# Performance work log

Measured on AMD Instinct MI355X. Metric: run time of the kernel, lower is better.

## Reference

```python
import jax, jax.numpy as jnp
import numpy as np

KERNEL = 7  # median blur window size (odd)


def setup_inputs() -> dict:
    key = jax.random.key(0)
    # NCHW image batch, values in [0,1) like normalized images
    img = jax.random.uniform(key, (8, 3, 512, 512), dtype=jnp.float32)
    return {"img": img}


def _median_blur(img, k):
    # Matches kornia.filters.median_blur: zero padding ('same'), then median
    # over the k*k window. k*k is odd so the exact middle of the sorted
    # window equals torch.median's lower median.
    pad = k // 2
    b, c, h, w = img.shape
    x = jnp.pad(img, ((0, 0), (0, 0), (pad, pad), (pad, pad)))  # zero pad
    # unfold: [B, C, k*k, H, W] — same materialization as kornia's conv2d
    # with binary one-hot kernels. Loop is over the fixed k*k = 49 taps.
    patches = jnp.stack(
        [x[:, :, i:i + h, j:j + w] for i in range(k) for j in range(k)],
        axis=2,
    )
    mid = (k * k) // 2
    return jnp.sort(patches, axis=2)[:, :, mid]  # [B, C, H, W]


def reference(img):
    return _median_blur(img, KERNEL)
```

## Files before the change

### kernel.cpp

```cpp
#include <hip/hip_runtime.h>
#include <utility>

#define IMG_H 512
#define IMG_W 512

typedef _Float16 h2 __attribute__((ext_vector_type(2)));

__device__ __forceinline__ h2 h2min(h2 a, h2 b) { return __builtin_elementwise_min(a, b); }
__device__ __forceinline__ h2 h2max(h2 a, h2 b) { return __builtin_elementwise_max(a, b); }

struct Op { int kind, a, b; };
constexpr int NSLOT = 352;
constexpr int MAXOPS = 4096;
constexpr int NCOLREG = 70;
struct Prog { Op ops[MAXOPS]; int n; int nphys; bool ok; bool noload; };

constexpr int pow2ceil(int x) { int p = 1; while (p < x) p += p; return p; }

struct Builder {
    Op ops[MAXOPS] = {};
    int n = 0;
    bool pad[NSLOT] = {};
    bool init[NSLOT] = {};
    bool ok = true;

    constexpr void emit(int k, int a, int b) {
        if (n < MAXOPS) ops[n++] = Op{k, a, b}; else ok = false;
    }
    constexpr void load(int s, int c) { emit(2, s, c); pad[s] = false; init[s] = true; }
    constexpr void mov(int d, int s) {
        if (!init[s] || d == s) ok = false;
        emit(1, d, s); pad[d] = pad[s]; init[d] = true;
    }
    constexpr void mkpad(int s) { pad[s] = true; init[s] = true; }
    constexpr void ce_(int a, int b) {
        if (!init[a] || !init[b]) { ok = false; return; }
        if (pad[a] && pad[b]) return;
        if (!pad[a] && pad[b]) return;
        if (pad[a] && !pad[b]) {
            emit(1, a, b); pad[a] = false; pad[b] = true; return;
        }
        emit(0, a, b);
    }
    constexpr void maxin(int a, int b) {
        if (!init[a] || !init[b] || pad[a] || pad[b]) ok = false;
        emit(5, a, b);
    }
    constexpr void minin(int a, int b) {
        if (!init[a] || !init[b] || pad[a] || pad[b]) ok = false;
        emit(4, a, b);
    }
    constexpr void sort_run(int base, int len) {
        for (int p = 1; p < len; p += p)
            for (int k = p; k > 0; k /= 2)
                for (int j = k % p; j + k < len; j += k + k)
                    for (int i = 0; i < k; ++i)
                        if (i + j + k < len)
                            if ((i + j) / (p + p) == (i + j + k) / (p + p))
                                ce_(base + i + j, base + i + j + k);
    }
    constexpr void merge_stage(int base, int P) {
        int nn = 2 * P, p = P;
        for (int k = p; k > 0; k /= 2)
            for (int j = k % p; j + k < nn; j += k + k)
                for (int i = 0; i < k; ++i) {
                    int a = i + j, b = i + j + k;
                    if (b < nn && a / (p + p) == b / (p + p)) ce_(base + a, base + b);
                }
    }
    constexpr void load_col(int base, int c) {
        for (int r = 0; r < 7; ++r) load(base + r, c * 7 + r);
        sort_run(base, 7);
    }
    constexpr void place(int dst, int src, int len, int P) {
        for (int i = 0; i < len; ++i) mov(dst + i, src + i);
        for (int i = len; i < P; ++i) mkpad(dst + i);
    }
    constexpr void merge_to(int dst, int s1, int l1, int s2, int l2) {
        int P = pow2ceil(l1 > l2 ? l1 : l2);
        place(dst, s1, l1, P);
        place(dst + P, s2, l2, P);
        merge_stage(dst, P);
    }
    constexpr void select_med49(int T, int A, int B, int o) {
        for (int t = 0; t < 7; ++t) {
            mov(T + t, A + 17 + t);
            maxin(B + 6 - t, T + t);
        }
        mov(T + 7, A + 24);
        minin(T, T + 1); minin(T + 2, T + 3);
        minin(T + 4, T + 5); minin(T + 6, T + 7);
        minin(T, T + 2); minin(T + 4, T + 6);
        minin(T, T + 4);
        if (!init[T] || pad[T]) ok = false;
        emit(3, o, T);
    }
};

constexpr Prog build() {
    Builder b{};
    constexpr int M12 = 112, M34 = 128, M56 = 144, M78 = 160;
    constexpr int C28A = 208, C42 = 272, T0 = 336, T1 = 344;

    for (int c = 1; c <= 8; ++c) b.load_col(8 * c, c);
    b.merge_to(M34, 8 * 3, 7, 8 * 4, 7);
    b.merge_to(M56, 8 * 5, 7, 8 * 6, 7);
    b.merge_to(C28A, M34, 14, M56, 14);
    b.merge_to(M12, 8 * 1, 7, 8 * 2, 7);
    b.merge_to(M78, 8 * 7, 7, 8 * 8, 7);

    b.merge_to(C42, C28A, 28, M12, 14);
    b.load_col(8 * 0, 0);
    b.select_med49(T0, C42, 8 * 0, 0);
    b.select_med49(T1, C42, 8 * 7, 1);

    b.merge_to(C42, C28A, 28, M78, 14);
    b.load_col(8 * 9, 9);
    b.select_med49(T0, C42, 8 * 2, 2);
    b.select_med49(T1, C42, 8 * 9, 3);

    Prog p{};
    bool needed[NSLOT] = {};
    int kindr[MAXOPS] = {};
    bool keep[MAXOPS] = {};
    for (int t = b.n - 1; t >= 0; --t) {
        Op o = b.ops[t];
        if (o.kind == 3) { keep[t] = true; kindr[t] = 3; needed[o.b] = true; }
        else if (o.kind == 0) {
            bool na = needed[o.a], nb = needed[o.b];
            if (na && nb)      { keep[t] = true; kindr[t] = 0; }
            else if (na)       { keep[t] = true; kindr[t] = 4; needed[o.b] = true; }
            else if (nb)       { keep[t] = true; kindr[t] = 5; needed[o.a] = true; }
        } else if (o.kind == 1) {
            if (needed[o.a]) { keep[t] = true; kindr[t] = 1; needed[o.a] = false; needed[o.b] = true; }
        } else if (o.kind == 2) {
            if (needed[o.a]) { keep[t] = true; kindr[t] = 2; needed[o.a] = false; }
        } else if (o.kind == 4) {
            if (needed[o.a]) { keep[t] = true; kindr[t] = 4; needed[o.b] = true; }
        } else if (o.kind == 5) {
            if (needed[o.b]) { keep[t] = true; kindr[t] = 5; needed[o.a] = true; }
        }
    }
    p.n = 0;
    for (int t = 0; t < b.n; ++t)
        if (keep[t]) { p.ops[p.n] = b.ops[t]; p.ops[p.n].kind = kindr[t]; ++p.n; }
    p.ok = b.ok;

    bool live[NSLOT] = {};
    bool lu_a[MAXOPS] = {};
    bool lu_b[MAXOPS] = {};
    for (int t = p.n - 1; t >= 0; --t) {
        Op o = p.ops[t];
        if (o.kind == 0 || o.kind == 4 || o.kind == 5) {
            lu_a[t] = !live[o.a]; lu_b[t] = !live[o.b];
        } else if (o.kind == 1 || o.kind == 3) {
            lu_b[t] = !live[o.b];
        }
        if (o.kind == 0) { live[o.a] = false; live[o.b] = false; }
        else if (o.kind == 1 || o.kind == 2 || o.kind == 4) live[o.a] = false;
        else if (o.kind == 5) live[o.b] = false;
        if (o.kind == 0 || o.kind == 4 || o.kind == 5) { live[o.a] = true; live[o.b] = true; }
        else if (o.kind == 1 || o.kind == 3) live[o.b] = true;
    }
    for (int t = 0; t < p.n; ++t) {
        Op o = p.ops[t];
        if (o.kind == 0 && (lu_a[t] || lu_b[t])) p.ok = false;
        if (o.kind == 4 && lu_a[t]) p.ok = false;
        if (o.kind == 5 && lu_b[t]) p.ok = false;
    }

    int phys[NSLOT] = {};
    bool bound[NSLOT] = {};
    bool claimed[NCOLREG] = {};
    int freelist[NSLOT] = {};
    bool drop[MAXOPS] = {};
    int nfree = 0, nphys = NCOLREG;
    for (int t = 0; t < p.n; ++t) {
        Op o = p.ops[t];
        if (o.kind == 0) {
            if (!bound[o.a] || !bound[o.b]) p.ok = false;
            p.ops[t].a = phys[o.a]; p.ops[t].b = phys[o.b];
        } else if (o.kind == 4) {
            if (!bound[o.a] || !bound[o.b]) p.ok = false;
            p.ops[t].a = phys[o.a]; p.ops[t].b = phys[o.b];
            if (lu_b[t]) { freelist[nfree++] = phys[o.b]; bound[o.b] = false; }
        } else if (o.kind == 5) {
            if (!bound[o.a] || !bound[o.b]) p.ok = false;
            p.ops[t].a = phys[o.a]; p.ops[t].b = phys[o.b];
            if (lu_a[t]) { freelist[nfree++] = phys[o.a]; bound[o.a] = false; }
        } else if (o.kind == 1) {
            if (!bound[o.b]) p.ok = false;
            int pb = phys[o.b];
            if (lu_b[t]) {
                if (bound[o.a]) { freelist[nfree++] = phys[o.a]; bound[o.a] = false; }
                phys[o.a] = pb; bound[o.a] = true; bound[o.b] = false;
                drop[t] = true;
            } else {
                p.ops[t].b = pb;
                if (bound[o.a]) { freelist[nfree++] = phys[o.a]; bound[o.a] = false; }
                int pa = (nfree > 0) ? freelist[--nfree] : nphys++;
                phys[o.a] = pa; bound[o.a] = true;
                p.ops[t].a = pa;
            }
        } else if (o.kind == 2) {
            if (o.b < 0 || o.b >= NCOLREG || claimed[o.b]) p.ok = false;
            else claimed[o.b] = true;
            if (bound[o.a]) { freelist[nfree++] = phys[o.a]; bound[o.a] = false; }
            phys[o.a] = o.b; bound[o.a] = true;
            drop[t] = true;
        } else {
            if (!bound[o.b]) p.ok = false;
            p.ops[t].b = phys[o.b];
            if (lu_b[t]) { freelist[nfree++] = phys[o.b]; bound[o.b] = false; }
        }
        if (nphys > NSLOT || nfree > NSLOT) p.ok = false;
    }
    p.nphys = nphys;

    int m = 0;
    p.noload = true;
    for (int t = 0; t < p.n; ++t) {
        if (drop[t]) continue;
        if (p.ops[t].kind == 2) p.noload = false;
        p.ops[m++] = p.ops[t];
    }
    p.n = m;
    return p;
}

constexpr Prog PROG = build();
static_assert(PROG.ok && PROG.n > 0 && PROG.n < 2000, "program build failed");
static_assert(PROG.noload, "a load op survived precoloring");
static_assert(PROG.nphys >= NCOLREG && PROG.nphys <= 256, "regalloc blew up");
constexpr int NPHYS = PROG.nphys;

template <int I>
__device__ __forceinline__ void step(h2* v, h2* med) {
    constexpr Op o = PROG.ops[I];
    if constexpr (o.kind == 0) {
        h2 lo = h2min(v[o.a], v[o.b]);
        h2 hi = h2max(v[o.a], v[o.b]);
        v[o.a] = lo; v[o.b] = hi;
    } else if constexpr (o.kind == 1) v[o.a] = v[o.b];
    else if constexpr (o.kind == 3) med[o.a] = v[o.b];
    else if constexpr (o.kind == 4) v[o.a] = h2min(v[o.a], v[o.b]);
    else v[o.b] = h2max(v[o.a], v[o.b]);
}

template <size_t... Is>
__device__ __forceinline__ void run_all(h2* v, h2* med, std::index_sequence<Is...>) {
    (step<(int)Is>(v, med), ...);
}

__global__ __launch_bounds__(256, 2) void median7x7_kernel(
        const float* __restrict__ img, float* __restrict__ out) {
    const int bc = blockIdx.z;
    const int tx = threadIdx.x;
    const int ty = threadIdx.y;
    const int x0 = (blockIdx.x * 64 + tx) * 4;
    const int y  = (blockIdx.y * 4 + ty) * 2;

    const float* base = img + (size_t)bc * (IMG_H * IMG_W);
    const bool okl = (x0 >= 4);
    const bool okr = (x0 <= 504);
    const int xl = okl ? (x0 - 4) : 0;
    const int xr = okr ? (x0 + 4) : 504;

    h2 v[NPHYS];
    float prv[10];
#pragma unroll
    for (int r = 0; r < 8; ++r) {
        const int yy = y - 3 + r;
        float4 Q0, Q1, Q2;
        if ((unsigned)yy < IMG_H) {
            const float* rp = base + (size_t)yy * IMG_W;
            Q0 = *(const float4*)(rp + xl);
            Q1 = *(const float4*)(rp + x0);
            Q2 = *(const float4*)(rp + xr);
        } else {
            Q0 = make_float4(0.f, 0.f, 0.f, 0.f); Q1 = Q0; Q2 = Q0;
        }
        float cur[10];
        cur[0] = okl ? Q0.y : 0.f; cur[1] = okl ? Q0.z : 0.f; cur[2] = okl ? Q0.w : 0.f;
        cur[3] = Q1.x; cur[4] = Q1.y; cur[5] = Q1.z; cur[6] = Q1.w;
        cur[7] = okr ? Q2.x : 0.f; cur[8] = okr ? Q2.y : 0.f; cur[9] = okr ? Q2.z : 0.f;
        if (r > 0) {
#pragma unroll
            for (int c = 0; c < 10; ++c)
                v[c * 7 + (r - 1)] = (h2)__builtin_amdgcn_cvt_pkrtz(prv[c], cur[c]);
        }
#pragma unroll
        for (int c = 0; c < 10; ++c) prv[c] = cur[c];
    }

    h2 med[4];
    run_all(v, med, std::make_index_sequence<(size_t)PROG.n>{});

    float* op = out + (size_t)bc * (IMG_H * IMG_W) + (size_t)y * IMG_W + x0;
    *(float4*)op = make_float4((float)med[0].x, (float)med[1].x,
                               (float)med[2].x, (float)med[3].x);
    *(float4*)(op + IMG_W) = make_float4((float)med[0].y, (float)med[1].y,
                                         (float)med[2].y, (float)med[3].y);
}

extern "C" void kernel_launch(void* const* d_in, const int* in_sizes, int n_in,
                              void* d_out, int out_size, void* d_ws, size_t ws_size,
                              hipStream_t stream) {
    const float* img = (const float*)d_in[0];
    float* out = (float*)d_out;
    dim3 grid(2, 64, 24);
    dim3 block(64, 4, 1);
    hipLaunchKernelGGL(median7x7_kernel, grid, block, 0, stream, img, out);
}
```

Baseline: 93.88 us.

## Shrink per-thread tile to 2x2 outputs to cut registers and raise occupancy

Each thread now computes 2 columns × 2 rows of medians instead of 4×2. The compile-time sorting-network program is rebuilt around 8 loaded columns with shared merges across the two outputs. Launch bounds rise to 4 blocks per SM and the grid doubles in x. This lowers register pressure and raises occupancy, but gives up the reuse of the shared 42-element merged column set across four outputs, so each output costs more sorting work.

New measurement: 105.6 us. 12.5% more time.

```diff
diff --git a/kernel.cpp b/kernel.cpp
--- a/kernel.cpp
+++ b/kernel.cpp
@@ -12,7 +12,7 @@
 struct Op { int kind, a, b; };
 constexpr int NSLOT = 352;
 constexpr int MAXOPS = 4096;
-constexpr int NCOLREG = 70;
+constexpr int NCOLREG = 56;
 struct Prog { Op ops[MAXOPS]; int n; int nphys; bool ok; bool noload; };
 
 constexpr int pow2ceil(int x) { int p = 1; while (p < x) p += p; return p; }
@@ -99,25 +99,20 @@
 
 constexpr Prog build() {
     Builder b{};
-    constexpr int M12 = 112, M34 = 128, M56 = 144, M78 = 160;
-    constexpr int C28A = 208, C42 = 272, T0 = 336, T1 = 344;
-
-    for (int c = 1; c <= 8; ++c) b.load_col(8 * c, c);
+    constexpr int M12 = 64, M34 = 80, M56 = 96;
+    constexpr int C28 = 120, C42 = 152, T0 = 220, T1 = 232;
+
+    for (int c = 1; c <= 6; ++c) b.load_col(8 * c, c);
     b.merge_to(M34, 8 * 3, 7, 8 * 4, 7);
     b.merge_to(M56, 8 * 5, 7, 8 * 6, 7);
-    b.merge_to(C28A, M34, 14, M56, 14);
+    b.merge_to(C28, M34, 14, M56, 14);
     b.merge_to(M12, 8 * 1, 7, 8 * 2, 7);
-    b.merge_to(M78, 8 * 7, 7, 8 * 8, 7);
-
-    b.merge_to(C42, C28A, 28, M12, 14);
+    b.merge_to(C42, C28, 28, M12, 14);
+
     b.load_col(8 * 0, 0);
     b.select_med49(T0, C42, 8 * 0, 0);
+    b.load_col(8 * 7, 7);
     b.select_med49(T1, C42, 8 * 7, 1);
-
-    b.merge_to(C42, C28A, 28, M78, 14);
-    b.load_col(8 * 9, 9);
-    b.select_med49(T0, C42, 8 * 2, 2);
-    b.select_med49(T1, C42, 8 * 9, 3);
 
     Prog p{};
     bool needed[NSLOT] = {};
@@ -231,7 +226,7 @@
 constexpr Prog PROG = build();
 static_assert(PROG.ok && PROG.n > 0 && PROG.n < 2000, "program build failed");
 static_assert(PROG.noload, "a load op survived precoloring");
-static_assert(PROG.nphys >= NCOLREG && PROG.nphys <= 256, "regalloc blew up");
+static_assert(PROG.nphys >= NCOLREG && PROG.nphys <= 160, "regalloc blew up");
 constexpr int NPHYS = PROG.nphys;
 
 template <int I>
@@ -252,55 +247,61 @@
     (step<(int)Is>(v, med), ...);
 }
 
-__global__ __launch_bounds__(256, 2) void median7x7_kernel(
+__global__ __launch_bounds__(256, 4) void median7x7_kernel(
         const float* __restrict__ img, float* __restrict__ out) {
     const int bc = blockIdx.z;
     const int tx = threadIdx.x;
     const int ty = threadIdx.y;
-    const int x0 = (blockIdx.x * 64 + tx) * 4;
+    const int x0 = (blockIdx.x * 64 + tx) * 2;
     const int y  = (blockIdx.y * 4 + ty) * 2;
 
     const float* base = img + (size_t)bc * (IMG_H * IMG_W);
-    const bool okl = (x0 >= 4);
-    const bool okr = (x0 <= 504);
-    const int xl = okl ? (x0 - 4) : 0;
-    const int xr = okr ? (x0 + 4) : 504;
+    const bool okA = (x0 >= 4);
+    const bool okB = (x0 >= 2);
+    const bool okD = (x0 <= 508);
+    const bool okE = (x0 <= 506);
+    const int xa = okA ? (x0 - 4) : 0;
+    const int xb = okB ? (x0 - 2) : 0;
+    const int xd = okD ? (x0 + 2) : 508;
+    const int xe = okE ? (x0 + 4) : 506;
 
     h2 v[NPHYS];
-    float prv[10];
+    float prv[8];
 #pragma unroll
     for (int r = 0; r < 8; ++r) {
         const int yy = y - 3 + r;
-        float4 Q0, Q1, Q2;
+        float2 A, B, C, D, E;
         if ((unsigned)yy < IMG_H) {
             const float* rp = base + (size_t)yy * IMG_W;
-            Q0 = *(const float4*)(rp + xl);
-            Q1 = *(const float4*)(rp + x0);
-            Q2 = *(const float4*)(rp + xr);
+            A = *(const float2*)(rp + xa);
+            B = *(const float2*)(rp + xb);
+            C = *(const float2*)(rp + x0);
+            D = *(const float2*)(rp + xd);
+            E = *(const float2*)(rp + xe);
         } else {
-            Q0 = make_float4(0.f, 0.f, 0.f, 0.f); Q1 = Q0; Q2 = Q0;
-        }
-        float cur[10];
-        cur[0] = okl ? Q0.y : 0.f; cur[1] = okl ? Q0.z : 0.f; cur[2] = okl ? Q0.w : 0.f;
-        cur[3] = Q1.x; cur[4] = Q1.y; cur[5] = Q1.z; cur[6] = Q1.w;
-        cur[7] = okr ? Q2.x : 0.f; cur[8] = okr ? Q2.y : 0.f; cur[9] = okr ? Q2.z : 0.f;
+            A = make_float2(0.f, 0.f); B = A; C = A; D = A; E = A;
+        }
+        float cur[8];
+        cur[0] = okA ? A.y : 0.f;
+        cur[1] = okB ? B.x : 0.f; cur[2] = okB ? B.y : 0.f;
+        cur[3] = C.x; cur[4] = C.y;
+        cur[5] = okD ? D.x : 0.f; cur[6] = okD ? D.y : 0.f;
+        cur[7] = okE ? E.x : 0.f;
         if (r > 0) {
 #pragma unroll
-            for (int c = 0; c < 10; ++c)
+            for (int c = 0; c < 8; ++c)
                 v[c * 7 + (r - 1)] = (h2)__builtin_amdgcn_cvt_pkrtz(prv[c], cur[c]);
         }
 #pragma unroll
-        for (int c = 0; c < 10; ++c) prv[c] = cur[c];
-    }
-
-    h2 med[4];
+        for (int c = 0; c < 8; ++c) prv[c] = cur[c];
+    }
+
+    h2 med[2];
     run_all(v, med, std::make_index_sequence<(size_t)PROG.n>{});
 
     float* op = out + (size_t)bc * (IMG_H * IMG_W) + (size_t)y * IMG_W + x0;
-    *(float4*)op = make_float4((float)med[0].x, (float)med[1].x,
-                               (float)med[2].x, (float)med[3].x);
-    *(float4*)(op + IMG_W) = make_float4((float)med[0].y, (float)med[1].y,
-                                         (float)med[2].y, (float)med[3].y);
+    *(float2*)op = make_float2((float)med[0].x, (float)med[1].x);
+    *(float2*)(op + IMG_W) = make_float2((float)med[0].y, (float)med[1].y);
 }
 
 extern "C" void kernel_launch(void* const* d_in, const int* in_sizes, int n_in,
@@ -308,7 +309,7 @@
                               hipStream_t stream) {
     const float* img = (const float*)d_in[0];
     float* out = (float*)d_out;
-    dim3 grid(2, 64, 24);
+    dim3 grid(4, 64, 24);
     dim3 block(64, 4, 1);
     hipLaunchKernelGGL(median7x7_kernel, grid, block, 0, stream, img, out);
 }
```
